# Kernel optimization log

Hardware: AMD Instinct MI355X
Metric: run time of the kernel (lower is better)

## Reference

```python
import jax, jax.numpy as jnp
import numpy as np

DIM = 192
HEADS = 6
HD = DIM // HEADS
WS = 7
R = 128  # low-rank projected sequence length
N_FULL = 3136  # 56*56
B = 32


def setup_inputs() -> dict:
    key = jax.random.key(0)
    ks = jax.random.split(key, 9)
    s = 0.02
    return {
        "x": jax.random.normal(ks[0], (2048, WS * WS, DIM), dtype=jnp.float32),
        "qkv_w": jax.random.normal(ks[1], (3 * DIM, DIM), dtype=jnp.float32) * s,
        "qkv_b": jax.random.normal(ks[2], (3 * DIM,), dtype=jnp.float32) * s,
        "E_w": jax.random.normal(ks[3], (R, N_FULL), dtype=jnp.float32) * s,
        "E_b": jax.random.normal(ks[4], (R,), dtype=jnp.float32) * s,
        "F_w": jax.random.normal(ks[5], (R, N_FULL), dtype=jnp.float32) * s,
        "F_b": jax.random.normal(ks[6], (R,), dtype=jnp.float32) * s,
        "proj_w": jax.random.normal(ks[7], (DIM, DIM), dtype=jnp.float32) * s,
        "proj_b": jax.random.normal(ks[8], (DIM,), dtype=jnp.float32) * s,
        "h": 56,
        "w": 56,
    }


def reference(x, qkv_w, qkv_b, E_w, E_b, F_w, F_b, proj_w, proj_b, h, w):
    C = x.shape[-1]
    # window_reverse: (nW*B, ws*ws, C) -> (B, H*W, C)
    xw = x.reshape(-1, WS, WS, C)
    b = xw.shape[0] // ((h // WS) * (w // WS))
    xm = xw.reshape(b, h // WS, w // WS, WS, WS, C)
    xm = xm.transpose(0, 1, 3, 2, 4, 5).reshape(b, h * w, C)
    n = h * w
    scale = 1.0 / np.sqrt(HD)

    qkv = (xm @ qkv_w.T + qkv_b).reshape(b, n, 3, HEADS, HD)
    qkv = qkv.transpose(2, 0, 3, 1, 4)  # (3, b, heads, n, hd)
    q, k, v = qkv[0] * scale, qkv[1], qkv[2]

    # Linformer low-rank projection along sequence: (b,h,n,d) -> (b,h,R,d)
    k_low = jnp.einsum('bhnd,kn->bhkd', k, E_w) + E_b[None, None, :, None]
    v_low = jnp.einsum('bhnd,kn->bhkd', v, F_w) + F_b[None, None, :, None]

    attn = jnp.einsum('bhnd,bhkd->bhnk', q, k_low)  # (b, heads, n, R)
    attn = jax.nn.softmax(attn, axis=-1)

    out = jnp.einsum('bhnk,bhkd->bhnd', attn, v_low)
    out = out.transpose(0, 2, 1, 3).reshape(b, n, C)
    out = out @ proj_w.T + proj_b
    return out
```

## Files before the change

### kernel.cpp

```cpp
#include <hip/hip_runtime.h>

typedef __bf16 bf16;
typedef bf16 bf16x8 __attribute__((ext_vector_type(8)));
typedef float f32x4 __attribute__((ext_vector_type(4)));

#define MFMA16(a,b,c) __builtin_amdgcn_mfma_f32_16x16x32_bf16(a,b,c,0,0,0)

#define NSEQ 3136
#define CDIM 192

__device__ inline bf16x8 cvt8(float4 a, float4 b) {
  bf16x8 r;
  r[0]=(bf16)a.x; r[1]=(bf16)a.y; r[2]=(bf16)a.z; r[3]=(bf16)a.w;
  r[4]=(bf16)b.x; r[5]=(bf16)b.y; r[6]=(bf16)b.z; r[7]=(bf16)b.w;
  return r;
}

__global__ void k_convert(const float* __restrict__ qkv_w, const float* __restrict__ E_w,
                          const float* __restrict__ F_w, const float* __restrict__ proj_w,
                          bf16* __restrict__ qkvw, bf16* __restrict__ EF, bf16* __restrict__ projw) {
  int i = blockIdx.x * blockDim.x + threadIdx.x;
  const int tot = 950272;
  for (; i < tot; i += gridDim.x * blockDim.x) {
    if (i < 110592) qkvw[i] = (bf16)qkv_w[i];
    else if (i < 512000) EF[i - 110592] = (bf16)E_w[i - 110592];
    else if (i < 913408) EF[i - 110592] = (bf16)F_w[i - 512000];
    else projw[i - 913408] = (bf16)proj_w[i - 913408];
  }
}

__global__ void k_rowsum(const float* __restrict__ E_w, const float* __restrict__ F_w,
                         float* __restrict__ rowsums) {
  __shared__ float red[4];
  int row = blockIdx.x;
  const float* src = (row < 128) ? (E_w + (long)row * NSEQ) : (F_w + (long)(row - 128) * NSEQ);
  float s = 0.f;
  for (int i = threadIdx.x; i < NSEQ; i += 256) s += src[i];
  for (int off = 32; off; off >>= 1) s += __shfl_xor(s, off);
  if ((threadIdx.x & 63) == 0) red[threadIdx.x >> 6] = s;
  __syncthreads();
  if (threadIdx.x == 0) rowsums[row] = red[0] + red[1] + red[2] + red[3];
}

__global__ void k_xT(const float* __restrict__ x, bf16* __restrict__ xmT) {
  __shared__ bf16 tile[32][200];
  int blk = blockIdx.x;
  int b = blk / 98, n0 = (blk % 98) * 32;
  int c = threadIdx.x;
  for (int i = 0; i < 32; ++i) {
    int n = n0 + i;
    int r = n / 56, cc = n % 56;
    long srcrow = ((long)(b * 64 + (r / 7) * 8 + (cc / 7)) * 49 + (r % 7) * 7 + (cc % 7));
    tile[i][c] = (bf16)x[srcrow * 192 + c];
  }
  __syncthreads();
  int nn = threadIdx.x & 31;
  int cb = threadIdx.x >> 5;
  for (int i = 0; i < 32; ++i) {
    int c2 = cb + 6 * i;
    xmT[((long)b * 192 + c2) * NSEQ + n0 + nn] = tile[nn][c2];
  }
}

__launch_bounds__(256)
__global__ void k_xlow(const bf16* __restrict__ EF, const bf16* __restrict__ xmT,
                       float* __restrict__ partial) {
  __shared__ bf16 As[64][72];
  __shared__ bf16 Bs[64][72];
  int idx = blockIdx.x;
  int s = idx % 7;
  int rem = (idx / 7) % 12;
  int b = idx / 84;
  int m0 = (rem / 3) * 64, n0 = (rem % 3) * 64;
  int kbase = s * 448;
  int tid = threadIdx.x;
  int wid = tid >> 6, lane = tid & 63;
  int wm = wid >> 1, wn = wid & 1;
  int lrow = lane & 15, lk = (lane >> 4) * 8;
  int srow = tid >> 2, skoff = (tid & 3) * 16;
  const bf16* Ap = EF + (long)(m0 + srow) * NSEQ + kbase + skoff;
  const bf16* Bp = xmT + ((long)b * 192 + n0 + srow) * NSEQ + kbase + skoff;
  f32x4 zero = {0.f, 0.f, 0.f, 0.f};
  f32x4 acc[2][2];
  for (int i = 0; i < 2; i++) for (int j = 0; j < 2; j++) acc[i][j] = zero;
  for (int k0 = 0; k0 < 448; k0 += 64) {
    *(bf16x8*)&As[srow][skoff]     = *(const bf16x8*)(Ap + k0);
    *(bf16x8*)&As[srow][skoff + 8] = *(const bf16x8*)(Ap + k0 + 8);
    *(bf16x8*)&Bs[srow][skoff]     = *(const bf16x8*)(Bp + k0);
    *(bf16x8*)&Bs[srow][skoff + 8] = *(const bf16x8*)(Bp + k0 + 8);
    __syncthreads();
    for (int ks = 0; ks < 2; ks++) {
      bf16x8 af[2], bfv[2];
      for (int i = 0; i < 2; i++) af[i]  = *(bf16x8*)&As[wm * 32 + 16 * i + lrow][ks * 32 + lk];
      for (int j = 0; j < 2; j++) bfv[j] = *(bf16x8*)&Bs[wn * 32 + 16 * j + lrow][ks * 32 + lk];
      for (int i = 0; i < 2; i++) for (int j = 0; j < 2; j++) acc[i][j] = MFMA16(af[i], bfv[j], acc[i][j]);
    }
    __syncthreads();
  }
  float* P = partial + (long)idx * 4096;
  for (int i = 0; i < 2; i++) for (int j = 0; j < 2; j++) for (int rr = 0; rr < 4; rr++) {
    int rl = wm * 32 + 16 * i + (lane >> 4) * 4 + rr;
    int cl = wn * 32 + 16 * j + lrow;
    P[rl * 64 + cl] = acc[i][j][rr];
  }
}

__global__ void k_reduce(const float* __restrict__ partial, bf16* __restrict__ el_fl) {
  int idx = blockIdx.x;
  int qtr = idx & 3;
  int bt = idx >> 2;
  int t = bt % 12, b = bt / 12;
  const float* P = partial + (long)bt * 7 * 4096 + qtr * 1024;
  for (int i = 0; i < 4; i++) {
    int e = i * 256 + threadIdx.x;
    float sum = 0.f;
    for (int s = 0; s < 7; s++) sum += P[s * 4096 + e];
    int ee = qtr * 1024 + e;
    int lm = ee >> 6, lc = ee & 63;
    int kr = (t / 3) * 64 + lm, c = (t % 3) * 64 + lc;
    el_fl[((long)b * 256 + kr) * 192 + c] = (bf16)sum;
  }
}

__launch_bounds__(256)
__global__ void k_lowproj(const bf16* __restrict__ el_fl, const bf16* __restrict__ qkvw,
                          const float* __restrict__ qkv_b, const float* __restrict__ E_b,
                          const float* __restrict__ F_b, const float* __restrict__ rowsums,
                          bf16* __restrict__ k_low, bf16* __restrict__ v_lowT) {
  __shared__ bf16 As[64][200];
  __shared__ bf16 Bs[64][200];
  int idx = blockIdx.x;
  int b = idx / 12, rem = idx % 12;
  int type = rem / 6; rem %= 6;
  int bm, bn;
  if (type == 0) { bm = rem / 3; bn = rem % 3; }
  else           { bm = rem / 2; bn = rem % 2; }
  int m0 = bm * 64, n0 = bn * 64;
  int tid = threadIdx.x;
  int wid = tid >> 6, lane = tid & 63;
  int wm = wid >> 1, wn = wid & 1;
  int lrow = lane & 15, lk = (lane >> 4) * 8;
  int srow = tid >> 2, skoff = (tid & 3) * 16;
  const bf16* Ap; const bf16* Bp;
  if (type == 0) {
    Ap = el_fl + ((long)b * 256 + m0 + srow) * 192 + skoff;
    Bp = qkvw + (long)(192 + n0 + srow) * 192 + skoff;
  } else {
    Ap = qkvw + (long)(384 + m0 + srow) * 192 + skoff;
    Bp = el_fl + ((long)b * 256 + 128 + n0 + srow) * 192 + skoff;
  }
  for (int kk = 0; kk < 192; kk += 64) {
    *(bf16x8*)&As[srow][kk + skoff]     = *(const bf16x8*)(Ap + kk);
    *(bf16x8*)&As[srow][kk + skoff + 8] = *(const bf16x8*)(Ap + kk + 8);
    *(bf16x8*)&Bs[srow][kk + skoff]     = *(const bf16x8*)(Bp + kk);
    *(bf16x8*)&Bs[srow][kk + skoff + 8] = *(const bf16x8*)(Bp + kk + 8);
  }
  __syncthreads();
  f32x4 zero = {0.f, 0.f, 0.f, 0.f};
  f32x4 acc[2][2];
  for (int i = 0; i < 2; i++) for (int j = 0; j < 2; j++) acc[i][j] = zero;
  for (int ks = 0; ks < 6; ks++) {
    bf16x8 af[2], bfv[2];
    for (int i = 0; i < 2; i++) af[i]  = *(bf16x8*)&As[wm * 32 + 16 * i + lrow][ks * 32 + lk];
    for (int j = 0; j < 2; j++) bfv[j] = *(bf16x8*)&Bs[wn * 32 + 16 * j + lrow][ks * 32 + lk];
    for (int i = 0; i < 2; i++) for (int j = 0; j < 2; j++) acc[i][j] = MFMA16(af[i], bfv[j], acc[i][j]);
  }
  if (type == 0) {
    for (int i = 0; i < 2; i++) for (int j = 0; j < 2; j++) for (int rr = 0; rr < 4; rr++) {
      int kr = m0 + wm * 32 + 16 * i + (lane >> 4) * 4 + rr;
      int c = n0 + wn * 32 + 16 * j + lrow;
      float v = acc[i][j][rr] + rowsums[kr] * qkv_b[192 + c] + E_b[kr];
      k_low[((long)b * 128 + kr) * 192 + c] = (bf16)v;
    }
  } else {
    for (int i = 0; i < 2; i++) for (int j = 0; j < 2; j++) for (int rr = 0; rr < 4; rr++) {
      int c = m0 + wm * 32 + 16 * i + (lane >> 4) * 4 + rr;
      int kr = n0 + wn * 32 + 16 * j + lrow;
      float v = acc[i][j][rr] + rowsums[128 + kr] * qkv_b[384 + c] + F_b[kr];
      v_lowT[((long)b * 192 + c) * 128 + kr] = (bf16)v;
    }
  }
}

__launch_bounds__(256)
__global__ void k_qgemm(const float* __restrict__ x, const bf16* __restrict__ qkvw,
                        const float* __restrict__ qkv_b, bf16* __restrict__ q) {
  __shared__ bf16 As[128][104];
  __shared__ bf16 Bs[192][104];
  long g0 = (long)blockIdx.x * 128;
  int tid = threadIdx.x;
  int wid = tid >> 6, lane = tid & 63;
  int lrow = lane & 15, lk = (lane >> 4) * 8;
  {
    int koff = (tid & 3) * 48;
    for (int r0 = 0; r0 < 192; r0 += 64) {
      int row = r0 + (tid >> 2);
      const bf16* Bp = qkvw + (long)row * 192 + koff;
      for (int m = 0; m < 6; m++)
        *(bf16x8*)&Bs[row][((koff + 8 * m) % 96) + (koff >= 96 ? 96 : 0)] = *(const bf16x8*)(Bp + 8 * m);
    }
  }
  int arow = tid >> 1, half = tid & 1;
  long g = g0 + arow;
  int b = (int)(g / NSEQ), n = (int)(g % NSEQ);
  int r = n / 56, cc = n % 56;
  long srcrow = (long)(b * 64 + (r / 7) * 8 + (cc / 7)) * 49 + (r % 7) * 7 + (cc % 7);
  const float* Ap = x + srcrow * 192 + half * 48;
  f32x4 zero = {0.f, 0.f, 0.f, 0.f};
  f32x4 acc[2][12];
  for (int i = 0; i < 2; i++) for (int j = 0; j < 12; j++) acc[i][j] = zero;
  for (int k0 = 0; k0 < 192; k0 += 96) {
    for (int m = 0; m < 3; m++) {
      const float4* xp = (const float4*)(Ap + k0 + 16 * m);
      float4 f0 = xp[0], f1 = xp[1];
      *(bf16x8*)&As[arow][half * 48 + 16 * m] = cvt8(f0, f1);
      float4 f2 = xp[2], f3 = xp[3];
      *(bf16x8*)&As[arow][half * 48 + 16 * m + 8] = cvt8(f2, f3);
    }
    __syncthreads();
    for (int ks = 0; ks < 3; ks++) {
      bf16x8 af[2];
      for (int i = 0; i < 2; i++) af[i] = *(bf16x8*)&As[wid * 32 + 16 * i + lrow][ks * 32 + lk];
      for (int j = 0; j < 12; j++) {
        bf16x8 bfv = *(bf16x8*)&Bs[16 * j + lrow][(k0 / 2) + ks * 16 + (lk / 2) + (lk & 4) * 12];
        (void)bfv;
      }
      for (int j = 0; j < 12; j++) {
        bf16x8 bv = *(bf16x8*)&Bs[16 * j + lrow][0];
        (void)bv;
      }
      (void)ks;
    }
    __syncthreads();
  }
  for (int i = 0; i < 2; i++) for (int j = 0; j < 12; j++) acc[i][j] = zero;
  __syncthreads();
  for (int k0 = 0; k0 < 192; k0 += 96) {
    for (int m = 0; m < 3; m++) {
      const float4* xp = (const float4*)(Ap + k0 + 16 * m);
      float4 f0 = xp[0], f1 = xp[1];
      *(bf16x8*)&As[arow][half * 48 + 16 * m] = cvt8(f0, f1);
      float4 f2 = xp[2], f3 = xp[3];
      *(bf16x8*)&As[arow][half * 48 + 16 * m + 8] = cvt8(f2, f3);
    }
    __syncthreads();
    for (int ks = 0; ks < 3; ks++) {
      bf16x8 af[2];
      for (int i = 0; i < 2; i++) af[i] = *(bf16x8*)&As[wid * 32 + 16 * i + lrow][ks * 32 + lk];
      for (int j = 0; j < 12; j++) {
        bf16x8 bv = *(bf16x8*)&Bs[16 * j + lrow][k0 + ks * 32 + lk - k0 + (k0 ? 0 : 0)];
        (void)bv;
      }
    }
    __syncthreads();
  }
  (void)acc;
}

__launch_bounds__(256)
__global__ void k_qgemm2(const float* __restrict__ x, const bf16* __restrict__ qkvw,
                         const float* __restrict__ qkv_b, bf16* __restrict__ q) {
  __shared__ bf16 As[128][104];
  __shared__ bf16 Bs[192][200];
  long g0 = (long)blockIdx.x * 128;
  int tid = threadIdx.x;
  int wid = tid >> 6, lane = tid & 63;
  int lrow = lane & 15, lk = (lane >> 4) * 8;
  {
    int koff = (tid & 3) * 48;
    for (int r0 = 0; r0 < 192; r0 += 64) {
      int row = r0 + (tid >> 2);
      const bf16* Bp = qkvw + (long)row * 192 + koff;
      for (int m = 0; m < 6; m++)
        *(bf16x8*)&Bs[row][koff + 8 * m] = *(const bf16x8*)(Bp + 8 * m);
    }
  }
  int arow = tid >> 1, half = tid & 1;
  long g = g0 + arow;
  int b = (int)(g / NSEQ), n = (int)(g % NSEQ);
  int r = n / 56, cc = n % 56;
  long srcrow = (long)(b * 64 + (r / 7) * 8 + (cc / 7)) * 49 + (r % 7) * 7 + (cc % 7);
  const float* Ap = x + srcrow * 192 + half * 48;
  f32x4 zero = {0.f, 0.f, 0.f, 0.f};
  f32x4 acc[2][12];
  for (int i = 0; i < 2; i++) for (int j = 0; j < 12; j++) acc[i][j] = zero;
  for (int k0 = 0; k0 < 192; k0 += 96) {
    for (int m = 0; m < 3; m++) {
      const float4* xp = (const float4*)(Ap + k0 + 16 * m);
      float4 f0 = xp[0], f1 = xp[1];
      float4 f2 = xp[2], f3 = xp[3];
      *(bf16x8*)&As[arow][half * 48 + 16 * m] = cvt8(f0, f1);
      *(bf16x8*)&As[arow][half * 48 + 16 * m + 8] = cvt8(f2, f3);
    }
    __syncthreads();
    for (int ks = 0; ks < 3; ks++) {
      bf16x8 af[2];
      for (int i = 0; i < 2; i++) af[i] = *(bf16x8*)&As[wid * 32 + 16 * i + lrow][ks * 32 + lk];
      for (int j = 0; j < 12; j++) {
        bf16x8 bv = *(bf16x8*)&Bs[16 * j + lrow][k0 + ks * 32 + lk];
        acc[0][j] = MFMA16(af[0], bv, acc[0][j]);
        acc[1][j] = MFMA16(af[1], bv, acc[1][j]);
      }
    }
    __syncthreads();
  }
  const float scale = 0.17677669529663687f;
  for (int i = 0; i < 2; i++) for (int j = 0; j < 12; j++) for (int rr = 0; rr < 4; rr++) {
    long grow = g0 + wid * 32 + 16 * i + (lane >> 4) * 4 + rr;
    int c = 16 * j + lrow;
    float v = (acc[i][j][rr] + qkv_b[c]) * scale;
    q[grow * 192 + c] = (bf16)v;
  }
}

__launch_bounds__(256)
__global__ void k_attn(const bf16* __restrict__ q, const bf16* __restrict__ k_low,
                       const bf16* __restrict__ v_lowT, bf16* __restrict__ out_att) {
  __shared__ bf16 Ks[128][40];
  __shared__ bf16 Vs[32][136];
  __shared__ bf16 Ps[4][16][136];
  int idx = blockIdx.x;
  int nt = idx % 49, bh = idx / 49;
  int h = bh % 6, b = bh / 6;
  int n0 = nt * 64;
  int tid = threadIdx.x;
  int wid = tid >> 6, lane = tid & 63;
  int lrow = lane & 15, lk = (lane >> 4) * 8;
  {
    int row = tid >> 1, koff = (tid & 1) * 16;
    const bf16* src = k_low + ((long)b * 128 + row) * 192 + h * 32 + koff;
    *(bf16x8*)&Ks[row][koff] = *(const bf16x8*)src;
    *(bf16x8*)&Ks[row][koff + 8] = *(const bf16x8*)(src + 8);
  }
  {
    int row = tid >> 3, koff = (tid & 7) * 16;
    const bf16* src = v_lowT + ((long)b * 192 + h * 32 + row) * 128 + koff;
    *(bf16x8*)&Vs[row][koff] = *(const bf16x8*)src;
    *(bf16x8*)&Vs[row][koff + 8] = *(const bf16x8*)(src + 8);
  }
  int nrow = n0 + wid * 16 + lrow;
  bf16x8 qf = *(const bf16x8*)(q + ((long)b * NSEQ + nrow) * 192 + h * 32 + lk);
  __syncthreads();
  f32x4 zero = {0.f, 0.f, 0.f, 0.f};
  f32x4 s[8];
  for (int f = 0; f < 8; f++) {
    bf16x8 kf = *(bf16x8*)&Ks[16 * f + lrow][lk];
    s[f] = MFMA16(qf, kf, zero);
  }
  for (int rr = 0; rr < 4; rr++) {
    float m = s[0][rr];
    for (int f = 1; f < 8; f++) m = fmaxf(m, s[f][rr]);
    for (int off = 1; off < 16; off <<= 1) m = fmaxf(m, __shfl_xor(m, off));
    float sum = 0.f;
    for (int f = 0; f < 8; f++) { float p = __expf(s[f][rr] - m); s[f][rr] = p; sum += p; }
    for (int off = 1; off < 16; off <<= 1) sum += __shfl_xor(sum, off);
    float inv = 1.0f / sum;
    for (int f = 0; f < 8; f++) s[f][rr] *= inv;
  }
  for (int f = 0; f < 8; f++)
    for (int rr = 0; rr < 4; rr++)
      Ps[wid][(lane >> 4) * 4 + rr][16 * f + lrow] = (bf16)s[f][rr];
  __syncthreads();
  f32x4 o[2];
  o[0] = zero; o[1] = zero;
  for (int ks = 0; ks < 4; ks++) {
    bf16x8 pf = *(bf16x8*)&Ps[wid][lrow][ks * 32 + lk];
    for (int j = 0; j < 2; j++) {
      bf16x8 vf = *(bf16x8*)&Vs[16 * j + lrow][ks * 32 + lk];
      o[j] = MFMA16(pf, vf, o[j]);
    }
  }
  for (int j = 0; j < 2; j++) for (int rr = 0; rr < 4; rr++) {
    int nn = n0 + wid * 16 + (lane >> 4) * 4 + rr;
    out_att[((long)b * NSEQ + nn) * 192 + h * 32 + 16 * j + lrow] = (bf16)o[j][rr];
  }
}

__launch_bounds__(256)
__global__ void k_proj(const bf16* __restrict__ oa, const bf16* __restrict__ projw,
                       const float* __restrict__ proj_b, float* __restrict__ out) {
  __shared__ bf16 As[128][104];
  __shared__ bf16 Bs[192][200];
  long g0 = (long)blockIdx.x * 128;
  int tid = threadIdx.x;
  int wid = tid >> 6, lane = tid & 63;
  int lrow = lane & 15, lk = (lane >> 4) * 8;
  {
    int koff = (tid & 3) * 48;
    for (int r0 = 0; r0 < 192; r0 += 64) {
      int row = r0 + (tid >> 2);
      const bf16* Bp = projw + (long)row * 192 + koff;
      for (int m = 0; m < 6; m++)
        *(bf16x8*)&Bs[row][koff + 8 * m] = *(const bf16x8*)(Bp + 8 * m);
    }
  }
  int arow = tid >> 1, half = tid & 1;
  const bf16* Ap = oa + (g0 + arow) * 192 + half * 48;
  f32x4 zero = {0.f, 0.f, 0.f, 0.f};
  f32x4 acc[2][12];
  for (int i = 0; i < 2; i++) for (int j = 0; j < 12; j++) acc[i][j] = zero;
  for (int k0 = 0; k0 < 192; k0 += 96) {
    for (int m = 0; m < 6; m++)
      *(bf16x8*)&As[arow][half * 48 + 8 * m] = *(const bf16x8*)(Ap + k0 + 8 * m);
    __syncthreads();
    for (int ks = 0; ks < 3; ks++) {
      bf16x8 af[2];
      for (int i = 0; i < 2; i++) af[i] = *(bf16x8*)&As[wid * 32 + 16 * i + lrow][ks * 32 + lk];
      for (int j = 0; j < 12; j++) {
        bf16x8 bv = *(bf16x8*)&Bs[16 * j + lrow][k0 + ks * 32 + lk];
        acc[0][j] = MFMA16(af[0], bv, acc[0][j]);
        acc[1][j] = MFMA16(af[1], bv, acc[1][j]);
      }
    }
    __syncthreads();
  }
  for (int i = 0; i < 2; i++) for (int j = 0; j < 12; j++) for (int rr = 0; rr < 4; rr++) {
    long grow = g0 + wid * 32 + 16 * i + (lane >> 4) * 4 + rr;
    int c = 16 * j + lrow;
    out[grow * 192 + c] = acc[i][j][rr] + proj_b[c];
  }
}

extern "C" void kernel_launch(void* const* d_in, const int* in_sizes, int n_in,
                              void* d_out, int out_size, void* d_ws, size_t ws_size,
                              hipStream_t stream) {
  const float* x      = (const float*)d_in[0];
  const float* qkv_w  = (const float*)d_in[1];
  const float* qkv_b  = (const float*)d_in[2];
  const float* E_w    = (const float*)d_in[3];
  const float* E_b    = (const float*)d_in[4];
  const float* F_w    = (const float*)d_in[5];
  const float* F_b    = (const float*)d_in[6];
  const float* proj_w = (const float*)d_in[7];
  const float* proj_b = (const float*)d_in[8];
  float* out = (float*)d_out;

  char* ws = (char*)d_ws;
  size_t off = 0;
  auto alloc = [&](size_t bytes) { char* p = ws + off; off += (bytes + 255) & ~(size_t)255; return p; };
  bf16* qkvw     = (bf16*)alloc((size_t)110592 * 2);
  bf16* EF       = (bf16*)alloc((size_t)802816 * 2);
  bf16* projw    = (bf16*)alloc((size_t)36864 * 2);
  float* rowsums = (float*)alloc((size_t)256 * 4);
  bf16* xmT      = (bf16*)alloc((size_t)32 * 192 * NSEQ * 2);
  float* partial = (float*)alloc((size_t)2688 * 4096 * 4);
  bf16* q        = (bf16*)partial;
  bf16* el_fl    = (bf16*)alloc((size_t)32 * 256 * 192 * 2);
  bf16* k_low    = (bf16*)alloc((size_t)32 * 128 * 192 * 2);
  bf16* v_lowT   = (bf16*)alloc((size_t)32 * 192 * 128 * 2);
  bf16* out_att  = xmT;

  k_convert<<<dim3(480), dim3(256), 0, stream>>>(qkv_w, E_w, F_w, proj_w, qkvw, EF, projw);
  k_rowsum<<<dim3(256), dim3(256), 0, stream>>>(E_w, F_w, rowsums);
  k_xT<<<dim3(32 * 98), dim3(192), 0, stream>>>(x, xmT);
  k_xlow<<<dim3(2688), dim3(256), 0, stream>>>(EF, xmT, partial);
  k_reduce<<<dim3(1536), dim3(256), 0, stream>>>(partial, el_fl);
  k_lowproj<<<dim3(384), dim3(256), 0, stream>>>(el_fl, qkvw, qkv_b, E_b, F_b, rowsums, k_low, v_lowT);
  k_qgemm2<<<dim3(784), dim3(256), 0, stream>>>(x, qkvw, qkv_b, q);
  k_attn<<<dim3(32 * 6 * 49), dim3(256), 0, stream>>>(q, k_low, v_lowT, out_att);
  k_proj<<<dim3(784), dim3(256), 0, stream>>>(out_att, projw, proj_b, out);
}
```

Baseline: 328.8 us.

## Fuse attention with output projection and vectorize window-transpose kernel

Merges the per-head attention kernel and the output projection GEMM into one kernel. Each block now loops over all six heads for a 64-row tile and keeps the attention output in shared memory before multiplying by proj_w. This removes the bf16 out_att round trip through global memory and one launch. K/V and projection weight fragments are now read straight from global/L2 instead of being staged in LDS. The transpose kernel now uses float4 loads and 8-wide bf16 stores over 64-row tiles. The dead k_qgemm kernel is deleted. The trade-off is fewer blocks (1568 vs 9408 for attention) and heavier per-block work, which may reduce parallelism.

```diff
diff --git a/kernel.cpp b/kernel.cpp
--- a/kernel.cpp
+++ b/kernel.cpp
@@ -2,6 +2,7 @@
 
 typedef __bf16 bf16;
 typedef bf16 bf16x8 __attribute__((ext_vector_type(8)));
+typedef bf16 bf16x4 __attribute__((ext_vector_type(4)));
 typedef float f32x4 __attribute__((ext_vector_type(4)));
 
 #define MFMA16(a,b,c) __builtin_amdgcn_mfma_f32_16x16x32_bf16(a,b,c,0,0,0)
@@ -43,22 +44,25 @@
 }
 
 __global__ void k_xT(const float* __restrict__ x, bf16* __restrict__ xmT) {
-  __shared__ bf16 tile[32][200];
+  __shared__ bf16 tile[64][196];
   int blk = blockIdx.x;
-  int b = blk / 98, n0 = (blk % 98) * 32;
-  int c = threadIdx.x;
-  for (int i = 0; i < 32; ++i) {
-    int n = n0 + i;
+  int b = blk / 49, n0 = (blk % 49) * 64;
+  int tid = threadIdx.x;
+  for (int e = tid; e < 3072; e += 256) {
+    int row = e / 48, c4 = e % 48;
+    int n = n0 + row;
     int r = n / 56, cc = n % 56;
-    long srcrow = ((long)(b * 64 + (r / 7) * 8 + (cc / 7)) * 49 + (r % 7) * 7 + (cc % 7));
-    tile[i][c] = (bf16)x[srcrow * 192 + c];
+    long srcrow = (long)(b * 64 + (r / 7) * 8 + (cc / 7)) * 49 + (r % 7) * 7 + (cc % 7);
+    float4 f = *(const float4*)(x + srcrow * 192 + c4 * 4);
+    bf16x4 v; v[0]=(bf16)f.x; v[1]=(bf16)f.y; v[2]=(bf16)f.z; v[3]=(bf16)f.w;
+    *(bf16x4*)&tile[row][c4 * 4] = v;
   }
   __syncthreads();
-  int nn = threadIdx.x & 31;
-  int cb = threadIdx.x >> 5;
-  for (int i = 0; i < 32; ++i) {
-    int c2 = cb + 6 * i;
-    xmT[((long)b * 192 + c2) * NSEQ + n0 + nn] = tile[nn][c2];
+  for (int e = tid; e < 1536; e += 256) {
+    int c = e >> 3, k = e & 7;
+    bf16x8 v;
+    for (int jj = 0; jj < 8; jj++) v[jj] = tile[k * 8 + jj][c];
+    *(bf16x8*)(xmT + ((long)b * 192 + c) * NSEQ + n0 + k * 8) = v;
   }
 }
 
@@ -180,81 +184,6 @@
       v_lowT[((long)b * 192 + c) * 128 + kr] = (bf16)v;
     }
   }
-}
-
-__launch_bounds__(256)
-__global__ void k_qgemm(const float* __restrict__ x, const bf16* __restrict__ qkvw,
-                        const float* __restrict__ qkv_b, bf16* __restrict__ q) {
-  __shared__ bf16 As[128][104];
-  __shared__ bf16 Bs[192][104];
-  long g0 = (long)blockIdx.x * 128;
-  int tid = threadIdx.x;
-  int wid = tid >> 6, lane = tid & 63;
-  int lrow = lane & 15, lk = (lane >> 4) * 8;
-  {
-    int koff = (tid & 3) * 48;
-    for (int r0 = 0; r0 < 192; r0 += 64) {
-      int row = r0 + (tid >> 2);
-      const bf16* Bp = qkvw + (long)row * 192 + koff;
-      for (int m = 0; m < 6; m++)
-        *(bf16x8*)&Bs[row][((koff + 8 * m) % 96) + (koff >= 96 ? 96 : 0)] = *(const bf16x8*)(Bp + 8 * m);
-    }
-  }
-  int arow = tid >> 1, half = tid & 1;
-  long g = g0 + arow;
-  int b = (int)(g / NSEQ), n = (int)(g % NSEQ);
-  int r = n / 56, cc = n % 56;
-  long srcrow = (long)(b * 64 + (r / 7) * 8 + (cc / 7)) * 49 + (r % 7) * 7 + (cc % 7);
-  const float* Ap = x + srcrow * 192 + half * 48;
-  f32x4 zero = {0.f, 0.f, 0.f, 0.f};
-  f32x4 acc[2][12];
-  for (int i = 0; i < 2; i++) for (int j = 0; j < 12; j++) acc[i][j] = zero;
-  for (int k0 = 0; k0 < 192; k0 += 96) {
-    for (int m = 0; m < 3; m++) {
-      const float4* xp = (const float4*)(Ap + k0 + 16 * m);
-      float4 f0 = xp[0], f1 = xp[1];
-      *(bf16x8*)&As[arow][half * 48 + 16 * m] = cvt8(f0, f1);
-      float4 f2 = xp[2], f3 = xp[3];
-      *(bf16x8*)&As[arow][half * 48 + 16 * m + 8] = cvt8(f2, f3);
-    }
-    __syncthreads();
-    for (int ks = 0; ks < 3; ks++) {
-      bf16x8 af[2];
-      for (int i = 0; i < 2; i++) af[i] = *(bf16x8*)&As[wid * 32 + 16 * i + lrow][ks * 32 + lk];
-      for (int j = 0; j < 12; j++) {
-        bf16x8 bfv = *(bf16x8*)&Bs[16 * j + lrow][(k0 / 2) + ks * 16 + (lk / 2) + (lk & 4) * 12];
-        (void)bfv;
-      }
-      for (int j = 0; j < 12; j++) {
-        bf16x8 bv = *(bf16x8*)&Bs[16 * j + lrow][0];
-        (void)bv;
-      }
-      (void)ks;
-    }
-    __syncthreads();
-  }
-  for (int i = 0; i < 2; i++) for (int j = 0; j < 12; j++) acc[i][j] = zero;
-  __syncthreads();
-  for (int k0 = 0; k0 < 192; k0 += 96) {
-    for (int m = 0; m < 3; m++) {
-      const float4* xp = (const float4*)(Ap + k0 + 16 * m);
-      float4 f0 = xp[0], f1 = xp[1];
-      *(bf16x8*)&As[arow][half * 48 + 16 * m] = cvt8(f0, f1);
-      float4 f2 = xp[2], f3 = xp[3];
-      *(bf16x8*)&As[arow][half * 48 + 16 * m + 8] = cvt8(f2, f3);
-    }
-    __syncthreads();
-    for (int ks = 0; ks < 3; ks++) {
-      bf16x8 af[2];
-      for (int i = 0; i < 2; i++) af[i] = *(bf16x8*)&As[wid * 32 + 16 * i + lrow][ks * 32 + lk];
-      for (int j = 0; j < 12; j++) {
-        bf16x8 bv = *(bf16x8*)&Bs[16 * j + lrow][k0 + ks * 32 + lk - k0 + (k0 ? 0 : 0)];
-        (void)bv;
-      }
-    }
-    __syncthreads();
-  }
-  (void)acc;
 }
 
 __launch_bounds__(256)
@@ -314,110 +243,78 @@
 }
 
 __launch_bounds__(256)
-__global__ void k_attn(const bf16* __restrict__ q, const bf16* __restrict__ k_low,
-                       const bf16* __restrict__ v_lowT, bf16* __restrict__ out_att) {
-  __shared__ bf16 Ks[128][40];
-  __shared__ bf16 Vs[32][136];
+__global__ void k_attnproj(const bf16* __restrict__ q, const bf16* __restrict__ k_low,
+                           const bf16* __restrict__ v_lowT, const bf16* __restrict__ projw,
+                           const float* __restrict__ proj_b, float* __restrict__ out) {
   __shared__ bf16 Ps[4][16][136];
+  __shared__ bf16 Os[64][200];
   int idx = blockIdx.x;
-  int nt = idx % 49, bh = idx / 49;
-  int h = bh % 6, b = bh / 6;
+  int nt = idx % 49, b = idx / 49;
   int n0 = nt * 64;
   int tid = threadIdx.x;
   int wid = tid >> 6, lane = tid & 63;
-  int lrow = lane & 15, lk = (lane >> 4) * 8;
+  int lrow = lane & 15, hi = lane >> 4;
+  int lk = hi * 8;
+  int nrow = n0 + wid * 16 + lrow;
+  bf16x8 qf[6];
   {
-    int row = tid >> 1, koff = (tid & 1) * 16;
-    const bf16* src = k_low + ((long)b * 128 + row) * 192 + h * 32 + koff;
-    *(bf16x8*)&Ks[row][koff] = *(const bf16x8*)src;
-    *(bf16x8*)&Ks[row][koff + 8] = *(const bf16x8*)(src + 8);
-  }
-  {
-    int row = tid >> 3, koff = (tid & 7) * 16;
-    const bf16* src = v_lowT + ((long)b * 192 + h * 32 + row) * 128 + koff;
-    *(bf16x8*)&Vs[row][koff] = *(const bf16x8*)src;
-    *(bf16x8*)&Vs[row][koff + 8] = *(const bf16x8*)(src + 8);
-  }
-  int nrow = n0 + wid * 16 + lrow;
-  bf16x8 qf = *(const bf16x8*)(q + ((long)b * NSEQ + nrow) * 192 + h * 32 + lk);
+    const bf16* qp = q + ((long)b * NSEQ + nrow) * 192 + lk;
+    for (int h = 0; h < 6; h++) qf[h] = *(const bf16x8*)(qp + h * 32);
+  }
+  f32x4 zero = {0.f, 0.f, 0.f, 0.f};
+  const bf16* kbase = k_low + ((long)b * 128 + lrow) * 192 + lk;
+  const bf16* vbase = v_lowT + ((long)b * 192 + lrow) * 128 + lk;
+  for (int h = 0; h < 6; h++) {
+    f32x4 s[8];
+    const bf16* kp = kbase + h * 32;
+    for (int f = 0; f < 8; f++)
+      s[f] = MFMA16(qf[h], *(const bf16x8*)(kp + (long)f * 16 * 192), zero);
+    for (int rr = 0; rr < 4; rr++) {
+      float m = s[0][rr];
+      for (int f = 1; f < 8; f++) m = fmaxf(m, s[f][rr]);
+      for (int off = 1; off < 16; off <<= 1) m = fmaxf(m, __shfl_xor(m, off));
+      float sum = 0.f;
+      for (int f = 0; f < 8; f++) { float p = __expf(s[f][rr] - m); s[f][rr] = p; sum += p; }
+      for (int off = 1; off < 16; off <<= 1) sum += __shfl_xor(sum, off);
+      float inv = 1.0f / sum;
+      for (int f = 0; f < 8; f++) s[f][rr] *= inv;
+    }
+    __syncthreads();
+    for (int f = 0; f < 8; f++)
+      for (int rr = 0; rr < 4; rr++)
+        Ps[wid][hi * 4 + rr][16 * f + lrow] = (bf16)s[f][rr];
+    __syncthreads();
+    f32x4 o[2]; o[0] = zero; o[1] = zero;
+    const bf16* vp = vbase + (long)h * 32 * 128;
+    for (int ks = 0; ks < 4; ks++) {
+      bf16x8 pf = *(bf16x8*)&Ps[wid][lrow][ks * 32 + lk];
+      for (int j = 0; j < 2; j++) {
+        bf16x8 vf = *(const bf16x8*)(vp + (long)j * 16 * 128 + ks * 32);
+        o[j] = MFMA16(pf, vf, o[j]);
+      }
+    }
+    for (int j = 0; j < 2; j++)
+      for (int rr = 0; rr < 4; rr++)
+        Os[wid * 16 + hi * 4 + rr][h * 32 + 16 * j + lrow] = (bf16)o[j][rr];
+  }
   __syncthreads();
-  f32x4 zero = {0.f, 0.f, 0.f, 0.f};
-  f32x4 s[8];
-  for (int f = 0; f < 8; f++) {
-    bf16x8 kf = *(bf16x8*)&Ks[16 * f + lrow][lk];
-    s[f] = MFMA16(qf, kf, zero);
-  }
-  for (int rr = 0; rr < 4; rr++) {
-    float m = s[0][rr];
-    for (int f = 1; f < 8; f++) m = fmaxf(m, s[f][rr]);
-    for (int off = 1; off < 16; off <<= 1) m = fmaxf(m, __shfl_xor(m, off));
-    float sum = 0.f;
-    for (int f = 0; f < 8; f++) { float p = __expf(s[f][rr] - m); s[f][rr] = p; sum += p; }
-    for (int off = 1; off < 16; off <<= 1) sum += __shfl_xor(sum, off);
-    float inv = 1.0f / sum;
-    for (int f = 0; f < 8; f++) s[f][rr] *= inv;
-  }
-  for (int f = 0; f < 8; f++)
-    for (int rr = 0; rr < 4; rr++)
-      Ps[wid][(lane >> 4) * 4 + rr][16 * f + lrow] = (bf16)s[f][rr];
-  __syncthreads();
-  f32x4 o[2];
-  o[0] = zero; o[1] = zero;
-  for (int ks = 0; ks < 4; ks++) {
-    bf16x8 pf = *(bf16x8*)&Ps[wid][lrow][ks * 32 + lk];
-    for (int j = 0; j < 2; j++) {
-      bf16x8 vf = *(bf16x8*)&Vs[16 * j + lrow][ks * 32 + lk];
-      o[j] = MFMA16(pf, vf, o[j]);
-    }
-  }
-  for (int j = 0; j < 2; j++) for (int rr = 0; rr < 4; rr++) {
-    int nn = n0 + wid * 16 + (lane >> 4) * 4 + rr;
-    out_att[((long)b * NSEQ + nn) * 192 + h * 32 + 16 * j + lrow] = (bf16)o[j][rr];
-  }
-}
-
-__launch_bounds__(256)
-__global__ void k_proj(const bf16* __restrict__ oa, const bf16* __restrict__ projw,
-                       const float* __restrict__ proj_b, float* __restrict__ out) {
-  __shared__ bf16 As[128][104];
-  __shared__ bf16 Bs[192][200];
-  long g0 = (long)blockIdx.x * 128;
-  int tid = threadIdx.x;
-  int wid = tid >> 6, lane = tid & 63;
-  int lrow = lane & 15, lk = (lane >> 4) * 8;
-  {
-    int koff = (tid & 3) * 48;
-    for (int r0 = 0; r0 < 192; r0 += 64) {
-      int row = r0 + (tid >> 2);
-      const bf16* Bp = projw + (long)row * 192 + koff;
-      for (int m = 0; m < 6; m++)
-        *(bf16x8*)&Bs[row][koff + 8 * m] = *(const bf16x8*)(Bp + 8 * m);
-    }
-  }
-  int arow = tid >> 1, half = tid & 1;
-  const bf16* Ap = oa + (g0 + arow) * 192 + half * 48;
-  f32x4 zero = {0.f, 0.f, 0.f, 0.f};
-  f32x4 acc[2][12];
-  for (int i = 0; i < 2; i++) for (int j = 0; j < 12; j++) acc[i][j] = zero;
-  for (int k0 = 0; k0 < 192; k0 += 96) {
-    for (int m = 0; m < 6; m++)
-      *(bf16x8*)&As[arow][half * 48 + 8 * m] = *(const bf16x8*)(Ap + k0 + 8 * m);
-    __syncthreads();
-    for (int ks = 0; ks < 3; ks++) {
-      bf16x8 af[2];
-      for (int i = 0; i < 2; i++) af[i] = *(bf16x8*)&As[wid * 32 + 16 * i + lrow][ks * 32 + lk];
-      for (int j = 0; j < 12; j++) {
-        bf16x8 bv = *(bf16x8*)&Bs[16 * j + lrow][k0 + ks * 32 + lk];
-        acc[0][j] = MFMA16(af[0], bv, acc[0][j]);
-        acc[1][j] = MFMA16(af[1], bv, acc[1][j]);
-      }
-    }
-    __syncthreads();
-  }
-  for (int i = 0; i < 2; i++) for (int j = 0; j < 12; j++) for (int rr = 0; rr < 4; rr++) {
-    long grow = g0 + wid * 32 + 16 * i + (lane >> 4) * 4 + rr;
-    int c = 16 * j + lrow;
-    out[grow * 192 + c] = acc[i][j][rr] + proj_b[c];
+  f32x4 acc[12];
+  for (int j = 0; j < 12; j++) acc[j] = zero;
+  const bf16* wb = projw + (long)lrow * 192 + lk;
+  for (int ks = 0; ks < 6; ks++) {
+    bf16x8 af = *(bf16x8*)&Os[wid * 16 + lrow][ks * 32 + lk];
+    for (int j = 0; j < 12; j++) {
+      bf16x8 bv = *(const bf16x8*)(wb + (long)j * 16 * 192 + ks * 32);
+      acc[j] = MFMA16(af, bv, acc[j]);
+    }
+  }
+  for (int j = 0; j < 12; j++) {
+    int co = 16 * j + lrow;
+    float pb = proj_b[co];
+    for (int rr = 0; rr < 4; rr++) {
+      long grow = (long)b * NSEQ + n0 + wid * 16 + hi * 4 + rr;
+      out[grow * 192 + co] = acc[j][rr] + pb;
+    }
   }
 }
 
@@ -448,15 +345,13 @@
   bf16* el_fl    = (bf16*)alloc((size_t)32 * 256 * 192 * 2);
   bf16* k_low    = (bf16*)alloc((size_t)32 * 128 * 192 * 2);
   bf16* v_lowT   = (bf16*)alloc((size_t)32 * 192 * 128 * 2);
-  bf16* out_att  = xmT;
 
   k_convert<<<dim3(480), dim3(256), 0, stream>>>(qkv_w, E_w, F_w, proj_w, qkvw, EF, projw);
   k_rowsum<<<dim3(256), dim3(256), 0, stream>>>(E_w, F_w, rowsums);
-  k_xT<<<dim3(32 * 98), dim3(192), 0, stream>>>(x, xmT);
+  k_xT<<<dim3(32 * 49), dim3(256), 0, stream>>>(x, xmT);
   k_xlow<<<dim3(2688), dim3(256), 0, stream>>>(EF, xmT, partial);
   k_reduce<<<dim3(1536), dim3(256), 0, stream>>>(partial, el_fl);
   k_lowproj<<<dim3(384), dim3(256), 0, stream>>>(el_fl, qkvw, qkv_b, E_b, F_b, rowsums, k_low, v_lowT);
   k_qgemm2<<<dim3(784), dim3(256), 0, stream>>>(x, qkvw, qkv_b, q);
-  k_attn<<<dim3(32 * 6 * 49), dim3(256), 0, stream>>>(q, k_low, v_lowT, out_att);
-  k_proj<<<dim3(784), dim3(256), 0, stream>>>(out_att, projw, proj_b, out);
-}
+  k_attnproj<<<dim3(32 * 49), dim3(256), 0, stream>>>(q, k_low, v_lowT, projw, proj_b, out);
+}
```

New measurement: 468.9 us. +42.6%, slower.
